# Kernel tuning notes

Measured on AMD Instinct MI355X. Metric: run time of the kernel, lower is better.

The kernel has to match this reference:

```python
import jax, jax.numpy as jnp
import numpy as np

N = 50000      # nodes
E0 = 400000    # random edges (before self loops)
F_IN = 64      # in_channels == out_channels (required by the view in forward)
H = 2          # heads
C = 64         # per-head out_channels
B, T = 1, 8
NEG_SLOPE = 0.2


def setup_inputs() -> dict:
    key = jax.random.key(0)
    ks = jax.random.split(key, 7)
    self_loops = jnp.arange(N, dtype=jnp.int32)  # GATConv add_self_loops=True
    src = jnp.concatenate([jax.random.randint(ks[0], (E0,), 0, N, dtype=jnp.int32), self_loops])
    dst = jnp.concatenate([jax.random.randint(ks[1], (E0,), 0, N, dtype=jnp.int32), self_loops])
    h = jax.random.normal(ks[2], (B, N, T, F_IN), dtype=jnp.float32)
    glorot = float(np.sqrt(2.0 / (F_IN + H * C)))
    W = jax.random.normal(ks[3], (F_IN, H, C), dtype=jnp.float32) * glorot
    att_src = jax.random.normal(ks[4], (H, C), dtype=jnp.float32) * 0.1
    att_dst = jax.random.normal(ks[5], (H, C), dtype=jnp.float32) * 0.1
    bias = jax.random.normal(ks[6], (C,), dtype=jnp.float32) * 0.1
    return {"h": h, "src": src, "dst": dst, "W": W,
            "att_src": att_src, "att_dst": att_dst, "bias": bias}


def _gat_step(xt, src, dst, W, att_src, att_dst, bias, n_nodes):
    # xt: [N, F_in] node features for one timestep
    xl = jnp.einsum('nf,fhc->nhc', xt, W)               # [N, H, C]
    a_s = jnp.einsum('nhc,hc->nh', xl, att_src)          # source score per node
    a_d = jnp.einsum('nhc,hc->nh', xl, att_dst)          # dest score per node
    e = jax.nn.leaky_relu(a_s[src] + a_d[dst], NEG_SLOPE)  # [E, H]
    # segment softmax over incoming edges of each destination node
    emax = jax.ops.segment_max(e, dst, num_segments=n_nodes)
    ex = jnp.exp(e - emax[dst])
    denom = jax.ops.segment_sum(ex, dst, num_segments=n_nodes)
    alpha = ex / denom[dst]                              # [E, H]
    msg = alpha[:, :, None] * xl[src]                    # [E, H, C]
    out = jax.ops.segment_sum(msg, dst, num_segments=n_nodes)  # [N, H, C]
    out = out.mean(axis=1) + bias                        # concat=False: head mean
    return jax.nn.elu(out)


def reference(h, src, dst, W, att_src, att_dst, bias):
    Bn, Nn, Tn, Fin = h.shape
    # [B, N, T, F] -> [B*T, N, F] (matches h.transpose(1,2).view(-1, N, F))
    x = jnp.transpose(h, (0, 2, 1, 3)).reshape(Bn * Tn, Nn, Fin)

    def step(carry, xt):
        return carry, _gat_step(xt, src, dst, W, att_src, att_dst, bias, Nn)

    _, outs = jax.lax.scan(step, None, x)                # [B*T, N, C]
    out = outs.reshape(Bn, Tn, Nn, -1)
    return jnp.transpose(out, (0, 2, 1, 3))              # [B, N, T, C]
```

## Files before the change

### kernel.cpp

```cpp
#include <hip/hip_runtime.h>
#include <hip/hip_bf16.h>
#include <math.h>

#define T_STEPS 8
#define F_IN 64
#define HC 128
#define C_OUT 64
#define NEG_SLOPE 0.2f

typedef _Float16 half8 __attribute__((ext_vector_type(8)));
typedef _Float16 half2v __attribute__((ext_vector_type(2)));
typedef float f32x4 __attribute__((ext_vector_type(4)));

static __device__ __forceinline__ float dot2(half2v a, half2v b, float c) {
    return __builtin_amdgcn_fdot2(a, b, c, false);
}

__global__ void k_zero_i32(int* p, int n) {
    int i = blockIdx.x * blockDim.x + threadIdx.x;
    if (i < n) p[i] = 0;
}

__global__ void k_count(const int* __restrict__ dst, int* __restrict__ cnt, int E) {
    int e = blockIdx.x * blockDim.x + threadIdx.x;
    if (e < E) atomicAdd(&cnt[dst[e]], 1);
}

__global__ void k_scan1(int* data, int* bsum, int n) {
    __shared__ int tmp[256];
    int tid = threadIdx.x;
    int i = blockIdx.x * 256 + tid;
    int v = (i < n) ? data[i] : 0;
    tmp[tid] = v; __syncthreads();
    for (int off = 1; off < 256; off <<= 1) {
        int x = (tid >= off) ? tmp[tid - off] : 0;
        __syncthreads();
        tmp[tid] += x;
        __syncthreads();
    }
    if (i < n) data[i] = tmp[tid] - v;
    if (tid == 255) bsum[blockIdx.x] = tmp[255];
}

__global__ void k_scan2(int* bsum, int nb) {
    __shared__ int tmp[256];
    int tid = threadIdx.x;
    int v = (tid < nb) ? bsum[tid] : 0;
    tmp[tid] = v; __syncthreads();
    for (int off = 1; off < 256; off <<= 1) {
        int x = (tid >= off) ? tmp[tid - off] : 0;
        __syncthreads();
        tmp[tid] += x;
        __syncthreads();
    }
    if (tid < nb) bsum[tid] = tmp[tid] - v;
}

__global__ void k_scan3(int* data, const int* __restrict__ bsum, int* cursor, int n, int total) {
    int i = blockIdx.x * 256 + threadIdx.x;
    if (i < n) {
        int v = data[i] + bsum[i >> 8];
        data[i] = v;
        cursor[i] = v;
    }
    if (i == 0) data[n] = total;
}

__global__ void k_fill(const int* __restrict__ src, const int* __restrict__ dst,
                       int* __restrict__ cursor, int* __restrict__ csr_src, int E) {
    int e = blockIdx.x * blockDim.x + threadIdx.x;
    if (e < E) {
        int d = dst[e];
        int pos = atomicAdd(&cursor[d], 1);
        csr_src[pos] = src[e];
    }
}

__global__ void k_prep(const float* __restrict__ W, const float* __restrict__ att_src,
                       const float* __restrict__ att_dst,
                       _Float16* __restrict__ Wt, _Float16* __restrict__ WQt) {
    int b = blockIdx.x;
    int tid = threadIdx.x;
    if (b == 0) {
        int q = tid & 3, f = tid >> 2;
        const float* att = (q & 2) ? att_dst : att_src;
        int hh = q & 1;
        float s = 0.f;
        #pragma unroll 8
        for (int c = 0; c < 64; c++) s += W[f * HC + hh * 64 + c] * att[hh * 64 + c];
        WQt[q * 64 + f] = (_Float16)s;
    } else {
        int i = (b - 1) * 256 + tid;
        int ei = i >> 6, k = i & 63;
        Wt[i] = (_Float16)W[k * HC + (ei & 1) * 64 + (ei >> 1)];
    }
}

__global__ __launch_bounds__(256) void k_gemm(
    const float* __restrict__ h, const _Float16* __restrict__ Wt,
    const _Float16* __restrict__ WQt,
    _Float16* __restrict__ xlh, float* __restrict__ a_s, float* __restrict__ a_d,
    int N)
{
    __shared__ _Float16 smem[64 * 136];
    _Float16* sA   = smem;
    _Float16* sOut = smem;

    int tid = threadIdx.x;
    int t = blockIdx.y;
    int node0 = blockIdx.x * 64;
    int w = tid >> 6;
    int lane = tid & 63;
    int cl = lane & 15;
    int lg = lane >> 4;

    {
        int row = tid >> 2;
        int k0 = (tid & 3) * 16;
        int n = node0 + row;
        int nc = n < N ? n : N - 1;
        const float* hp = h + ((size_t)nc * T_STEPS + t) * F_IN + k0;
        f32x4 x0 = __builtin_nontemporal_load((const f32x4*)(hp));
        f32x4 x1 = __builtin_nontemporal_load((const f32x4*)(hp + 4));
        f32x4 x2 = __builtin_nontemporal_load((const f32x4*)(hp + 8));
        f32x4 x3 = __builtin_nontemporal_load((const f32x4*)(hp + 12));
        half8 p0, p1;
        p0[0] = (_Float16)x0[0]; p0[1] = (_Float16)x0[1];
        p0[2] = (_Float16)x0[2]; p0[3] = (_Float16)x0[3];
        p0[4] = (_Float16)x1[0]; p0[5] = (_Float16)x1[1];
        p0[6] = (_Float16)x1[2]; p0[7] = (_Float16)x1[3];
        p1[0] = (_Float16)x2[0]; p1[1] = (_Float16)x2[1];
        p1[2] = (_Float16)x2[2]; p1[3] = (_Float16)x2[3];
        p1[4] = (_Float16)x3[0]; p1[5] = (_Float16)x3[1];
        p1[6] = (_Float16)x3[2]; p1[7] = (_Float16)x3[3];
        *(half8*)&sA[row * 72 + k0]     = p0;
        *(half8*)&sA[row * 72 + k0 + 8] = p1;
    }
    __syncthreads();

    half8 af[4][2];
    #pragma unroll
    for (int rt = 0; rt < 4; rt++)
        #pragma unroll
        for (int ks = 0; ks < 2; ks++)
            af[rt][ks] = *(half8*)&sA[(rt * 16 + cl) * 72 + ks * 32 + lg * 8];

    half8 bf[2][2];
    #pragma unroll
    for (int ct = 0; ct < 2; ct++)
        #pragma unroll
        for (int ks = 0; ks < 2; ks++)
            bf[ct][ks] = *(const half8*)&Wt[(size_t)(w * 32 + ct * 16 + cl) * 64 + ks * 32 + lg * 8];

    half8 bq[2];
    #pragma unroll
    for (int ks = 0; ks < 2; ks++) {
        half8 b = {};
        if (cl < 4) b = *(const half8*)&WQt[cl * 64 + ks * 32 + lg * 8];
        bq[ks] = b;
    }

    __syncthreads();

    #pragma unroll
    for (int rt = 0; rt < 4; rt++)
        #pragma unroll
        for (int ct = 0; ct < 2; ct++) {
            f32x4 c = {0.f, 0.f, 0.f, 0.f};
            c = __builtin_amdgcn_mfma_f32_16x16x32_f16(af[rt][0], bf[ct][0], c, 0, 0, 0);
            c = __builtin_amdgcn_mfma_f32_16x16x32_f16(af[rt][1], bf[ct][1], c, 0, 0, 0);
            int slot = w * 32 + ct * 16 + cl;
            #pragma unroll
            for (int reg = 0; reg < 4; reg++)
                sOut[(rt * 16 + lg * 4 + reg) * 136 + slot] = (_Float16)c[reg];
        }

    f32x4 sacc = {0.f, 0.f, 0.f, 0.f};
    sacc = __builtin_amdgcn_mfma_f32_16x16x32_f16(af[w][0], bq[0], sacc, 0, 0, 0);
    sacc = __builtin_amdgcn_mfma_f32_16x16x32_f16(af[w][1], bq[1], sacc, 0, 0, 0);

    float* ast = a_s + (size_t)t * N * 2;
    float* adt = a_d + (size_t)t * N * 2;
    if (cl < 4) {
        float* basep = (cl & 2) ? adt : ast;
        #pragma unroll
        for (int reg = 0; reg < 4; reg++) {
            int n = node0 + w * 16 + lg * 4 + reg;
            if (n < N) basep[(size_t)n * 2 + (cl & 1)] = sacc[reg];
        }
    }

    __syncthreads();

    _Float16* xlt = xlh + (size_t)t * N * HC;
    #pragma unroll
    for (int it = 0; it < 4; it++) {
        int idx = it * 256 + tid;
        int row = idx >> 4;
        int seg = idx & 15;
        int n = node0 + row;
        if (n < N)
            *(half8*)&xlt[(size_t)n * HC + seg * 8] = *(half8*)&sOut[row * 136 + seg * 8];
    }
}

__global__ __launch_bounds__(256) void k_edge(
    const int* __restrict__ csr_row, const int* __restrict__ csr_src,
    const float* __restrict__ a_s, const float* __restrict__ a_d,
    const _Float16* __restrict__ xlh, const float* __restrict__ bias,
    float* __restrict__ out, int N)
{
    __shared__ int2 edata[16][34];

    int tid  = threadIdx.x;
    int lane = tid & 63;
    int wid  = tid >> 6;
    int grp  = lane >> 4;
    int gl   = lane & 15;
    int t = blockIdx.y;
    const _Float16* xlt = xlh + (size_t)t * N * HC;
    const char* xb = (const char*)xlt;
    const float* ast = a_s + (size_t)t * N * 2;
    const float* adt = a_d + (size_t)t * N * 2;

    int nodeBlock0 = blockIdx.x * 16;
    int node = nodeBlock0 + wid * 4 + grp;
    bool nvalid = node < N;

    int beg = 0, end = 0;
    if (nvalid) { beg = csr_row[node]; end = csr_row[node + 1]; }
    int deg = end - beg;

    if (__ballot(deg > 32) == 0ull) {
        float2 adv = make_float2(0.f, 0.f);
        if (nvalid) adv = *(const float2*)&adt[(size_t)node * 2];

        int ea = beg + gl, eb = beg + gl + 16;
        bool eva = nvalid && (ea < end);
        bool evb = nvalid && (eb < end);
        int sa = eva ? csr_src[ea] : 0;
        int sb = evb ? csr_src[eb] : 0;
        float ea0 = -1e30f, ea1 = -1e30f, eb0 = -1e30f, eb1 = -1e30f;
        if (eva) {
            float2 v = *(const float2*)&ast[(size_t)sa * 2];
            ea0 = v.x + adv.x; ea1 = v.y + adv.y;
            ea0 = ea0 > 0.f ? ea0 : NEG_SLOPE * ea0;
            ea1 = ea1 > 0.f ? ea1 : NEG_SLOPE * ea1;
        }
        if (evb) {
            float2 v = *(const float2*)&ast[(size_t)sb * 2];
            eb0 = v.x + adv.x; eb1 = v.y + adv.y;
            eb0 = eb0 > 0.f ? eb0 : NEG_SLOPE * eb0;
            eb1 = eb1 > 0.f ? eb1 : NEG_SLOPE * eb1;
        }
        float m0 = fmaxf(ea0, eb0), m1 = fmaxf(ea1, eb1);
        #pragma unroll
        for (int off = 8; off >= 1; off >>= 1) {
            m0 = fmaxf(m0, __shfl_xor(m0, off));
            m1 = fmaxf(m1, __shfl_xor(m1, off));
        }
        float xa0 = eva ? __expf(ea0 - m0) : 0.f;
        float xa1 = eva ? __expf(ea1 - m1) : 0.f;
        float xb0 = evb ? __expf(eb0 - m0) : 0.f;
        float xb1 = evb ? __expf(eb1 - m1) : 0.f;
        float d0 = xa0 + xb0, d1 = xa1 + xb1;
        #pragma unroll
        for (int off = 8; off >= 1; off >>= 1) {
            d0 += __shfl_xor(d0, off);
            d1 += __shfl_xor(d1, off);
        }
        float r0 = 0.5f / d0, r1 = 0.5f / d1;

        union { uint u; _Float16 hh[2]; } cwa, cwb;
        cwa.hh[0] = (_Float16)(xa0 * r0); cwa.hh[1] = (_Float16)(xa1 * r1);
        cwb.hh[0] = (_Float16)(xb0 * r0); cwb.hh[1] = (_Float16)(xb1 * r1);
        int myrow = wid * 4 + grp;
        edata[myrow][gl]      = make_int2(eva ? (sa << 8) : 0, (int)cwa.u);
        edata[myrow][gl + 16] = make_int2(evb ? (sb << 8) : 0, (int)cwb.u);

        int wmax = deg;
        wmax = max(wmax, __shfl_xor(wmax, 16));
        wmax = max(wmax, __shfl_xor(wmax, 32));
        int dkr = (wmax + 3) & ~3;

        const int2* row = edata[myrow];
        int sb16 = gl * 16;
        float ac0 = 0.f, ac1 = 0.f, ac2 = 0.f, ac3 = 0.f;
        union h8u { half8 v; half2v h[4]; };
        for (int j = 0; j < dkr; j += 4) {
            int4 p = *(const int4*)&row[j];
            int4 q = *(const int4*)&row[j + 2];
            h8u v0, v1, v2, v3;
            v0.v = *(const half8*)(xb + p.x + sb16);
            v1.v = *(const half8*)(xb + p.z + sb16);
            v2.v = *(const half8*)(xb + q.x + sb16);
            v3.v = *(const half8*)(xb + q.z + sb16);
            union { int i; half2v h; } w0, w1, w2, w3;
            w0.i = p.y; w1.i = p.w; w2.i = q.y; w3.i = q.w;
            ac0 = dot2(v0.h[0], w0.h, ac0);
            ac1 = dot2(v0.h[1], w0.h, ac1);
            ac2 = dot2(v0.h[2], w0.h, ac2);
            ac3 = dot2(v0.h[3], w0.h, ac3);
            ac0 = dot2(v1.h[0], w1.h, ac0);
            ac1 = dot2(v1.h[1], w1.h, ac1);
            ac2 = dot2(v1.h[2], w1.h, ac2);
            ac3 = dot2(v1.h[3], w1.h, ac3);
            ac0 = dot2(v2.h[0], w2.h, ac0);
            ac1 = dot2(v2.h[1], w2.h, ac1);
            ac2 = dot2(v2.h[2], w2.h, ac2);
            ac3 = dot2(v2.h[3], w2.h, ac3);
            ac0 = dot2(v3.h[0], w3.h, ac0);
            ac1 = dot2(v3.h[1], w3.h, ac1);
            ac2 = dot2(v3.h[2], w3.h, ac2);
            ac3 = dot2(v3.h[3], w3.h, ac3);
        }
        if (nvalid) {
            float4 bv = *(const float4*)&bias[gl * 4];
            float c0 = ac0 + bv.x, c1 = ac1 + bv.y, c2 = ac2 + bv.z, c3 = ac3 + bv.w;
            f32x4 o;
            o[0] = c0 > 0.f ? c0 : expm1f(c0);
            o[1] = c1 > 0.f ? c1 : expm1f(c1);
            o[2] = c2 > 0.f ? c2 : expm1f(c2);
            o[3] = c3 > 0.f ? c3 : expm1f(c3);
            __builtin_nontemporal_store(o,
                (f32x4*)&out[((size_t)node * T_STEPS + t) * C_OUT + gl * 4]);
        }
    } else {
        float bs = bias[lane];
        #pragma unroll
        for (int k = 0; k < 4; k++) {
            int nk = nodeBlock0 + wid * 4 + k;
            if (nk >= N) continue;
            int bk = __shfl(beg, k * 16);
            int ek = __shfl(end, k * 16);
            float2 adv = *(const float2*)&adt[(size_t)nk * 2];

            float m0 = -1e30f, m1 = -1e30f;
            for (int e = bk + lane; e < ek; e += 64) {
                int s = csr_src[e];
                float2 asv = *(const float2*)&ast[(size_t)s * 2];
                float e0 = asv.x + adv.x, e1 = asv.y + adv.y;
                e0 = e0 > 0.f ? e0 : NEG_SLOPE * e0;
                e1 = e1 > 0.f ? e1 : NEG_SLOPE * e1;
                m0 = fmaxf(m0, e0); m1 = fmaxf(m1, e1);
            }
            #pragma unroll
            for (int off = 32; off >= 1; off >>= 1) {
                m0 = fmaxf(m0, __shfl_xor(m0, off));
                m1 = fmaxf(m1, __shfl_xor(m1, off));
            }
            float d0 = 0.f, d1 = 0.f;
            for (int e = bk + lane; e < ek; e += 64) {
                int s = csr_src[e];
                float2 asv = *(const float2*)&ast[(size_t)s * 2];
                float e0 = asv.x + adv.x, e1 = asv.y + adv.y;
                e0 = e0 > 0.f ? e0 : NEG_SLOPE * e0;
                e1 = e1 > 0.f ? e1 : NEG_SLOPE * e1;
                d0 += __expf(e0 - m0); d1 += __expf(e1 - m1);
            }
            #pragma unroll
            for (int off = 32; off >= 1; off >>= 1) {
                d0 += __shfl_xor(d0, off);
                d1 += __shfl_xor(d1, off);
            }
            float r0 = 0.5f / d0, r1 = 0.5f / d1;

            float a0 = 0.f, a1 = 0.f;
            for (int base = bk; base < ek; base += 64) {
                int e = base + lane;
                int cnt = min(64, ek - base);
                int soff = 0;
                union { uint u; _Float16 hh[2]; } cw;
                cw.u = 0u;
                if (e < ek) {
                    int s = csr_src[e];
                    soff = s << 8;
                    float2 asv = *(const float2*)&ast[(size_t)s * 2];
                    float e0 = asv.x + adv.x, e1 = asv.y + adv.y;
                    e0 = e0 > 0.f ? e0 : NEG_SLOPE * e0;
                    e1 = e1 > 0.f ? e1 : NEG_SLOPE * e1;
                    cw.hh[0] = (_Float16)(__expf(e0 - m0) * r0);
                    cw.hh[1] = (_Float16)(__expf(e1 - m1) * r1);
                }
                int wv = (int)cw.u;
                for (int j = 0; j < cnt; j++) {
                    int sj = __shfl(soff, j);
                    int wj = __shfl(wv, j);
                    union { int i; half2v h; } c; c.i = wj;
                    half2v v = *(const half2v*)(xb + sj + lane * 4);
                    a0 = dot2(v, c.h, a0);
                }
            }
            float acc = a0 + a1 + bs;
            float o = acc > 0.f ? acc : expm1f(acc);
            __builtin_nontemporal_store(o, &out[((size_t)nk * T_STEPS + t) * C_OUT + lane]);
        }
    }
}

extern "C" void kernel_launch(void* const* d_in, const int* in_sizes, int n_in,
                              void* d_out, int out_size, void* d_ws, size_t ws_size,
                              hipStream_t stream)
{
    const float* h       = (const float*)d_in[0];
    const int*   src     = (const int*)d_in[1];
    const int*   dst     = (const int*)d_in[2];
    const float* W       = (const float*)d_in[3];
    const float* att_src = (const float*)d_in[4];
    const float* att_dst = (const float*)d_in[5];
    const float* bias    = (const float*)d_in[6];
    float* out = (float*)d_out;

    int N = in_sizes[0] / (T_STEPS * F_IN);
    int E = in_sizes[1];

    char* wsb = (char*)d_ws;
    size_t off = 0;
    auto alloc = [&](size_t bytes) -> char* {
        off = (off + 255) & ~(size_t)255;
        char* p = wsb + off;
        off += bytes;
        return p;
    };

    int* csr_row = (int*)alloc((size_t)(N + 1) * sizeof(int));
    int* cursor  = (int*)alloc((size_t)N * sizeof(int));
    int* bsum    = (int*)alloc(1024 * sizeof(int));
    int* csr_src = (int*)alloc((size_t)E * sizeof(int));
    float* a_s   = (float*)alloc((size_t)T_STEPS * N * 2 * sizeof(float));
    float* a_d   = (float*)alloc((size_t)T_STEPS * N * 2 * sizeof(float));
    _Float16* Wt  = (_Float16*)alloc((size_t)HC * 64 * sizeof(_Float16));
    _Float16* WQt = (_Float16*)alloc(4 * 64 * sizeof(_Float16));
    _Float16* xlh = (_Float16*)alloc((size_t)T_STEPS * N * HC * sizeof(_Float16));

    int nb = (N + 255) / 256;
    k_zero_i32<<<(N + 1 + 255) / 256, 256, 0, stream>>>(csr_row, N + 1);
    k_count<<<(E + 255) / 256, 256, 0, stream>>>(dst, csr_row, E);
    k_scan1<<<nb, 256, 0, stream>>>(csr_row, bsum, N);
    k_scan2<<<1, 256, 0, stream>>>(bsum, nb);
    k_scan3<<<nb, 256, 0, stream>>>(csr_row, bsum, cursor, N, E);
    k_fill<<<(E + 255) / 256, 256, 0, stream>>>(src, dst, cursor, csr_src, E);

    k_prep<<<33, 256, 0, stream>>>(W, att_src, att_dst, Wt, WQt);
    dim3 gg((N + 63) / 64, T_STEPS);
    k_gemm<<<gg, 256, 0, stream>>>(h, Wt, WQt, xlh, a_s, a_d, N);
    dim3 ge((N + 15) / 16, T_STEPS);
    k_edge<<<ge, 256, 0, stream>>>(csr_row, csr_src, a_s, a_d, xlh, bias, out, N);
}
```

Measured before the change: 418.5 us.

## Loop over timesteps inside GEMM block with double-buffered prefetch of next input

The projection GEMM kernel now processes all 8 timesteps in a single block instead of launching one block per timestep. The weight fragments are loaded once per block, and the next timestep's input rows are prefetched into a second shared-memory buffer while the current timestep's MFMAs run. This removes repeated weight loads and gives more contiguous reads of h per block. In exchange the grid shrinks eightfold, which lowers parallelism and occupancy, and each iteration adds barriers.

```diff
diff --git a/kernel.cpp b/kernel.cpp
--- a/kernel.cpp
+++ b/kernel.cpp
@@ -102,24 +102,38 @@
     _Float16* __restrict__ xlh, float* __restrict__ a_s, float* __restrict__ a_d,
     int N)
 {
-    __shared__ _Float16 smem[64 * 136];
-    _Float16* sA   = smem;
-    _Float16* sOut = smem;
+    __shared__ _Float16 sA[2][64 * 72];
+    __shared__ _Float16 sOut[64 * 136];
 
     int tid = threadIdx.x;
-    int t = blockIdx.y;
     int node0 = blockIdx.x * 64;
     int w = tid >> 6;
     int lane = tid & 63;
     int cl = lane & 15;
     int lg = lane >> 4;
 
+    int srow = tid >> 2;
+    int k0 = (tid & 3) * 16;
+    int sn = node0 + srow;
+    int snc = sn < N ? sn : N - 1;
+    const float* hp = h + (size_t)snc * (T_STEPS * F_IN) + k0;
+
+    half8 bf[2][2];
+    #pragma unroll
+    for (int ct = 0; ct < 2; ct++)
+        #pragma unroll
+        for (int ks = 0; ks < 2; ks++)
+            bf[ct][ks] = *(const half8*)&Wt[(size_t)(w * 32 + ct * 16 + cl) * 64 + ks * 32 + lg * 8];
+
+    half8 bq[2];
+    #pragma unroll
+    for (int ks = 0; ks < 2; ks++) {
+        half8 b = {};
+        if (cl < 4) b = *(const half8*)&WQt[cl * 64 + ks * 32 + lg * 8];
+        bq[ks] = b;
+    }
+
     {
-        int row = tid >> 2;
-        int k0 = (tid & 3) * 16;
-        int n = node0 + row;
-        int nc = n < N ? n : N - 1;
-        const float* hp = h + ((size_t)nc * T_STEPS + t) * F_IN + k0;
         f32x4 x0 = __builtin_nontemporal_load((const f32x4*)(hp));
         f32x4 x1 = __builtin_nontemporal_load((const f32x4*)(hp + 4));
         f32x4 x2 = __builtin_nontemporal_load((const f32x4*)(hp + 8));
@@ -133,74 +147,86 @@
         p1[2] = (_Float16)x2[2]; p1[3] = (_Float16)x2[3];
         p1[4] = (_Float16)x3[0]; p1[5] = (_Float16)x3[1];
         p1[6] = (_Float16)x3[2]; p1[7] = (_Float16)x3[3];
-        *(half8*)&sA[row * 72 + k0]     = p0;
-        *(half8*)&sA[row * 72 + k0 + 8] = p1;
+        *(half8*)&sA[0][srow * 72 + k0]     = p0;
+        *(half8*)&sA[0][srow * 72 + k0 + 8] = p1;
     }
     __syncthreads();
 
-    half8 af[4][2];
-    #pragma unroll
-    for (int rt = 0; rt < 4; rt++)
-        #pragma unroll
-        for (int ks = 0; ks < 2; ks++)
-            af[rt][ks] = *(half8*)&sA[(rt * 16 + cl) * 72 + ks * 32 + lg * 8];
-
-    half8 bf[2][2];
-    #pragma unroll
-    for (int ct = 0; ct < 2; ct++)
-        #pragma unroll
-        for (int ks = 0; ks < 2; ks++)
-            bf[ct][ks] = *(const half8*)&Wt[(size_t)(w * 32 + ct * 16 + cl) * 64 + ks * 32 + lg * 8];
-
-    half8 bq[2];
-    #pragma unroll
-    for (int ks = 0; ks < 2; ks++) {
-        half8 b = {};
-        if (cl < 4) b = *(const half8*)&WQt[cl * 64 + ks * 32 + lg * 8];
-        bq[ks] = b;
-    }
-
-    __syncthreads();
-
-    #pragma unroll
-    for (int rt = 0; rt < 4; rt++)
-        #pragma unroll
-        for (int ct = 0; ct < 2; ct++) {
-            f32x4 c = {0.f, 0.f, 0.f, 0.f};
-            c = __builtin_amdgcn_mfma_f32_16x16x32_f16(af[rt][0], bf[ct][0], c, 0, 0, 0);
-            c = __builtin_amdgcn_mfma_f32_16x16x32_f16(af[rt][1], bf[ct][1], c, 0, 0, 0);
-            int slot = w * 32 + ct * 16 + cl;
+    for (int t = 0; t < T_STEPS; t++) {
+        int p = t & 1;
+
+        half8 af[4][2];
+        #pragma unroll
+        for (int rt = 0; rt < 4; rt++)
             #pragma unroll
-            for (int reg = 0; reg < 4; reg++)
-                sOut[(rt * 16 + lg * 4 + reg) * 136 + slot] = (_Float16)c[reg];
-        }
-
-    f32x4 sacc = {0.f, 0.f, 0.f, 0.f};
-    sacc = __builtin_amdgcn_mfma_f32_16x16x32_f16(af[w][0], bq[0], sacc, 0, 0, 0);
-    sacc = __builtin_amdgcn_mfma_f32_16x16x32_f16(af[w][1], bq[1], sacc, 0, 0, 0);
-
-    float* ast = a_s + (size_t)t * N * 2;
-    float* adt = a_d + (size_t)t * N * 2;
-    if (cl < 4) {
-        float* basep = (cl & 2) ? adt : ast;
-        #pragma unroll
-        for (int reg = 0; reg < 4; reg++) {
-            int n = node0 + w * 16 + lg * 4 + reg;
-            if (n < N) basep[(size_t)n * 2 + (cl & 1)] = sacc[reg];
-        }
-    }
-
-    __syncthreads();
-
-    _Float16* xlt = xlh + (size_t)t * N * HC;
-    #pragma unroll
-    for (int it = 0; it < 4; it++) {
-        int idx = it * 256 + tid;
-        int row = idx >> 4;
-        int seg = idx & 15;
-        int n = node0 + row;
-        if (n < N)
-            *(half8*)&xlt[(size_t)n * HC + seg * 8] = *(half8*)&sOut[row * 136 + seg * 8];
+            for (int ks = 0; ks < 2; ks++)
+                af[rt][ks] = *(half8*)&sA[p][(rt * 16 + cl) * 72 + ks * 32 + lg * 8];
+
+        f32x4 x0, x1, x2, x3;
+        if (t < T_STEPS - 1) {
+            const float* hq = hp + (t + 1) * F_IN;
+            x0 = __builtin_nontemporal_load((const f32x4*)(hq));
+            x1 = __builtin_nontemporal_load((const f32x4*)(hq + 4));
+            x2 = __builtin_nontemporal_load((const f32x4*)(hq + 8));
+            x3 = __builtin_nontemporal_load((const f32x4*)(hq + 12));
+        }
+
+        __syncthreads();
+
+        #pragma unroll
+        for (int rt = 0; rt < 4; rt++)
+            #pragma unroll
+            for (int ct = 0; ct < 2; ct++) {
+                f32x4 c = {0.f, 0.f, 0.f, 0.f};
+                c = __builtin_amdgcn_mfma_f32_16x16x32_f16(af[rt][0], bf[ct][0], c, 0, 0, 0);
+                c = __builtin_amdgcn_mfma_f32_16x16x32_f16(af[rt][1], bf[ct][1], c, 0, 0, 0);
+                int slot = w * 32 + ct * 16 + cl;
+                #pragma unroll
+                for (int reg = 0; reg < 4; reg++)
+                    sOut[(rt * 16 + lg * 4 + reg) * 136 + slot] = (_Float16)c[reg];
+            }
+
+        f32x4 sacc = {0.f, 0.f, 0.f, 0.f};
+        sacc = __builtin_amdgcn_mfma_f32_16x16x32_f16(af[w][0], bq[0], sacc, 0, 0, 0);
+        sacc = __builtin_amdgcn_mfma_f32_16x16x32_f16(af[w][1], bq[1], sacc, 0, 0, 0);
+
+        if (t < T_STEPS - 1) {
+            half8 p0, p1;
+            p0[0] = (_Float16)x0[0]; p0[1] = (_Float16)x0[1];
+            p0[2] = (_Float16)x0[2]; p0[3] = (_Float16)x0[3];
+            p0[4] = (_Float16)x1[0]; p0[5] = (_Float16)x1[1];
+            p0[6] = (_Float16)x1[2]; p0[7] = (_Float16)x1[3];
+            p1[0] = (_Float16)x2[0]; p1[1] = (_Float16)x2[1];
+            p1[2] = (_Float16)x2[2]; p1[3] = (_Float16)x2[3];
+            p1[4] = (_Float16)x3[0]; p1[5] = (_Float16)x3[1];
+            p1[6] = (_Float16)x3[2]; p1[7] = (_Float16)x3[3];
+            *(half8*)&sA[p ^ 1][srow * 72 + k0]     = p0;
+            *(half8*)&sA[p ^ 1][srow * 72 + k0 + 8] = p1;
+        }
+
+        __syncthreads();
+
+        float* ast = a_s + (size_t)t * N * 2;
+        float* adt = a_d + (size_t)t * N * 2;
+        if (cl < 4) {
+            float* basep = (cl & 2) ? adt : ast;
+            #pragma unroll
+            for (int reg = 0; reg < 4; reg++) {
+                int n = node0 + w * 16 + lg * 4 + reg;
+                if (n < N) basep[(size_t)n * 2 + (cl & 1)] = sacc[reg];
+            }
+        }
+
+        _Float16* xlt = xlh + (size_t)t * N * HC;
+        #pragma unroll
+        for (int it = 0; it < 4; it++) {
+            int idx = it * 256 + tid;
+            int row = idx >> 4;
+            int seg = idx & 15;
+            int n = node0 + row;
+            if (n < N)
+                *(half8*)&xlt[(size_t)n * HC + seg * 8] = *(half8*)&sOut[row * 136 + seg * 8];
+        }
     }
 }
 
@@ -442,8 +468,7 @@
     k_fill<<<(E + 255) / 256, 256, 0, stream>>>(src, dst, cursor, csr_src, E);
 
     k_prep<<<33, 256, 0, stream>>>(W, att_src, att_dst, Wt, WQt);
-    dim3 gg((N + 63) / 64, T_STEPS);
-    k_gemm<<<gg, 256, 0, stream>>>(h, Wt, WQt, xlh, a_s, a_d, N);
+    k_gemm<<<(N + 63) / 64, 256, 0, stream>>>(h, Wt, WQt, xlh, a_s, a_d, N);
     dim3 ge((N + 15) / 16, T_STEPS);
     k_edge<<<ge, 256, 0, stream>>>(csr_row, csr_src, a_s, a_d, xlh, bias, out, N);
 }
```

Result: slower. 463.8 us (+10.8%).
